# Optimization experiments

Measured on AMD Instinct MI355X. Metric: run time of the kernel, lower is better.

## Reference

```python
import jax, jax.numpy as jnp
import numpy as np

# irreps_in = irreps_out = 64x0e + 32x1o
MUL0, MUL1 = 64, 32          # multiplicities of 0e scalars and 1o vectors
DIM_IN = MUL0 + MUL1 * 3     # 160
N_NODES = 50000
IU0, IV0 = np.triu_indices(MUL0, k=1)   # 2016 scalar u<v pairs
IU1, IV1 = np.triu_indices(MUL1, k=1)   # 496 vector u<v pairs
# e3nn path normalization (component / element):
#   i_out=0 (0e): num_elements sum = 2016 + 64 + 496 + 32 = 2608, dim(0e)=1
#   i_out=1 (1o): num_elements = 32*64 = 2048, dim(1o)=3
C0 = float(np.sqrt(1.0 / 2608.0))
C1 = float(np.sqrt(3.0 / 2048.0))
INV_SQRT3 = float(1.0 / np.sqrt(3.0))   # w3j(1,0,1) and w3j(1,1,0) CG factor


def setup_inputs() -> dict:
    key = jax.random.key(0)
    ks = jax.random.split(key, 7)
    node_feats = jax.random.normal(ks[0], (N_NODES, DIM_IN), jnp.float32)
    node_messages = jax.random.normal(ks[1], (N_NODES, DIM_IN), jnp.float32)
    W1 = jax.random.normal(ks[2], (len(IU0), MUL0), jnp.float32)  # (0e,0e)->0e u<vw
    W2 = jax.random.normal(ks[3], (MUL0, MUL0), jnp.float32)      # (0e,0e)->0e uuw
    W3 = jax.random.normal(ks[4], (MUL1, MUL0, MUL1), jnp.float32)  # (1o,0e)->1o uvw
    W4 = jax.random.normal(ks[5], (len(IU1), MUL0), jnp.float32)  # (1o,1o)->0e u<vw
    W5 = jax.random.normal(ks[6], (MUL1, MUL0), jnp.float32)      # (1o,1o)->0e uuw
    return {"node_feats": node_feats, "node_messages": node_messages,
            "W1": W1, "W2": W2, "W3": W3, "W4": W4, "W5": W5}


def _tensor_square(x, W1, W2, W3, W4, W5):
    x0 = x[:, :MUL0]                        # [N, 64] scalars (0e)
    x1 = x[:, MUL0:].reshape(-1, MUL1, 3)   # [N, 32, 3] vectors (1o)
    # (0e x 0e) -> 0e
    pair0 = x0[:, IU0] * x0[:, IV0]         # [N, 2016]
    sq0 = x0 * x0                           # [N, 64]
    # (1o x 1o) -> 0e via dot products (w3j(1,1,0) = delta/sqrt3)
    d = jnp.einsum('nui,nvi->nuv', x1, x1)  # [N, 32, 32]
    pair1 = d[:, IU1, IV1] * INV_SQRT3      # [N, 496]
    diag1 = jnp.einsum('nui,nui->nu', x1, x1) * INV_SQRT3  # [N, 32]
    out0 = C0 * (pair0 @ W1 + sq0 @ W2 + pair1 @ W4 + diag1 @ W5)  # [N, 64]
    # (1o x 0e) -> 1o fully connected uvw (w3j(1,0,1) = eye/sqrt3)
    out1 = (C1 * INV_SQRT3) * jnp.einsum('nui,nv,uvw->nwi', x1, x0, W3)  # [N,32,3]
    return jnp.concatenate([out0, out1.reshape(-1, MUL1 * 3)], axis=1)


def reference(node_feats, node_messages, W1, W2, W3, W4, W5):
    x = node_feats + node_messages
    return _tensor_square(x, W1, W2, W3, W4, W5)
```

## Files before the change

### kernel.cpp

```cpp
#include <hip/hip_runtime.h>

typedef unsigned short u16;
typedef unsigned int u32;

#define N_NODES 50000
#define NB      32

#define BG_OFF  0
#define BT_OFF  262144
#define BH_OFF  327680

#define ASTR   72
#define XTSTR  36

typedef __attribute__((ext_vector_type(8))) short short8;
typedef __attribute__((ext_vector_type(4))) float f32x4;
union U4S8 { uint4 u; short8 s; };

__device__ __forceinline__ u16 f2bf(float f) {
    u32 u = __float_as_uint(f);
    return (u16)((u + 0x7fffu + ((u >> 16) & 1u)) >> 16);
}
__device__ __forceinline__ f32x4 bf4(uint2 q) {
    f32x4 r;
    r[0] = __uint_as_float(q.x << 16);
    r[1] = __uint_as_float(q.x & 0xffff0000u);
    r[2] = __uint_as_float(q.y << 16);
    r[3] = __uint_as_float(q.y & 0xffff0000u);
    return r;
}

__global__ __launch_bounds__(256)
void pack_kernel(const float* __restrict__ W1, const float* __restrict__ W2,
                 const float* __restrict__ W3, const float* __restrict__ W4,
                 const float* __restrict__ W5, u16* __restrict__ ws) {
    const float INV_SQRT3 = 0.57735026918962576f;
    int T = blockIdx.x * 256 + threadIdx.x;
    int slot0 = T * 8;
    float vals[8];
    if (slot0 < BT_OFF) {
        int ntile = slot0 >> 10, rem = slot0 & 1023;
        int ks = rem >> 9, q = (rem & 511) >> 3;
        int vbase = ks * 32 + (q >> 4) * 8;
        int j = ntile * 16 + (q & 15);
        int u = j >> 6, w = j & 63;
        #pragma unroll
        for (int jj = 0; jj < 8; ++jj) {
            int v = vbase + jj;
            if (v == u) vals[jj] = W2[u * 64 + w];
            else {
                int a = min(u, v), b = max(u, v);
                int p = a * (127 - a) / 2 + (b - a - 1);
                vals[jj] = 0.5f * W1[p * 64 + w];
            }
        }
    } else if (slot0 < BH_OFF) {
        int s = slot0 - BT_OFF;
        int ntile = s >> 10, rem = s & 1023;
        int ks = rem >> 9, q = (rem & 511) >> 3;
        int vbase = ks * 32 + (q >> 4) * 8;
        int j = ntile * 16 + (q & 15);
        int u = j >> 5, w = j & 31;
        #pragma unroll
        for (int jj = 0; jj < 8; ++jj)
            vals[jj] = W3[(u * 64 + (vbase + jj)) * 32 + w];
    } else {
        int s = slot0 - BH_OFF;
        int ntile = s >> 9, q = (s & 511) >> 3;
        int vbase = (q >> 4) * 8;
        int j = ntile * 16 + (q & 15);
        int u = j >> 6, w = j & 63;
        #pragma unroll
        for (int jj = 0; jj < 8; ++jj) {
            int v = vbase + jj;
            if (v == u) vals[jj] = W5[u * 64 + w] * INV_SQRT3;
            else {
                int a = min(u, v), b = max(u, v);
                int p = a * (63 - a) / 2 + (b - a - 1);
                vals[jj] = (0.5f * INV_SQRT3) * W4[p * 64 + w];
            }
        }
    }
    uint4 o;
    o.x = ((u32)f2bf(vals[1]) << 16) | f2bf(vals[0]);
    o.y = ((u32)f2bf(vals[3]) << 16) | f2bf(vals[2]);
    o.z = ((u32)f2bf(vals[5]) << 16) | f2bf(vals[4]);
    o.w = ((u32)f2bf(vals[7]) << 16) | f2bf(vals[6]);
    *(uint4*)(ws + slot0) = o;
}

__global__ __launch_bounds__(256, 3)
void node_block_kernel(const float* __restrict__ feats, const float* __restrict__ msgs,
                       const u16* __restrict__ ws, float* __restrict__ out) {
    __shared__ u16 A_S[32 * ASTR];
    __shared__ u16 x0T[64 * XTSTR];
    __shared__ u16 x1T[96 * XTSTR];

    const int tid = threadIdx.x;
    const int node0 = blockIdx.x * NB;

    for (int k = 0; k < 3; ++k) {
        int chunk = tid + k * 256;
        if (chunk < 640) {
            int idx = chunk * 8;
            int n = (u32)idx / 160u;
            int d = idx - n * 160;
            int g = node0 * 160 + idx;
            float v[8];
            if (g + 8 <= N_NODES * 160) {
                float4 fa0 = *(const float4*)(feats + g);
                float4 fa1 = *(const float4*)(feats + g + 4);
                float4 fb0 = *(const float4*)(msgs + g);
                float4 fb1 = *(const float4*)(msgs + g + 4);
                v[0]=fa0.x+fb0.x; v[1]=fa0.y+fb0.y; v[2]=fa0.z+fb0.z; v[3]=fa0.w+fb0.w;
                v[4]=fa1.x+fb1.x; v[5]=fa1.y+fb1.y; v[6]=fa1.z+fb1.z; v[7]=fa1.w+fb1.w;
            } else {
                #pragma unroll
                for (int j = 0; j < 8; ++j) v[j] = 0.f;
            }
            u16 bv[8];
            #pragma unroll
            for (int j = 0; j < 8; ++j) bv[j] = f2bf(v[j]);
            if (d < 64) {
                uint4 pk;
                pk.x = ((u32)bv[1] << 16) | bv[0];
                pk.y = ((u32)bv[3] << 16) | bv[2];
                pk.z = ((u32)bv[5] << 16) | bv[4];
                pk.w = ((u32)bv[7] << 16) | bv[6];
                *(uint4*)&A_S[n * ASTR + d] = pk;
                #pragma unroll
                for (int j = 0; j < 8; ++j) x0T[(d + j) * XTSTR + n] = bv[j];
            } else {
                #pragma unroll
                for (int j = 0; j < 8; ++j)
                    x1T[(d + j - 64) * XTSTR + n] = bv[j];
            }
        }
    }
    __syncthreads();

    const int wave = tid >> 6, lane = tid & 63, quad = lane >> 4, l15 = lane & 15;
    const int wq = wave;
    const f32x4 z4 = {0.f, 0.f, 0.f, 0.f};
    const int ph64 = (blockIdx.x * 5) & 63;
    const int ph32 = (blockIdx.x * 5) & 31;

    f32x4 o0[2];
    #pragma unroll
    for (int mt = 0; mt < 2; ++mt) o0[mt] = z4;

    {
        short8 aS[2][2];
        #pragma unroll
        for (int mt = 0; mt < 2; ++mt)
            #pragma unroll
            for (int ks = 0; ks < 2; ++ks) {
                U4S8 t; t.u = *(const uint4*)&A_S[(mt * 16 + l15) * ASTR + ks * 32 + quad * 8];
                aS[mt][ks] = t.s;
            }
        const u16* bp = ws + BG_OFF + (u32)wq * 1024 + lane * 8;
        U4S8 b0[2], b1[2];
        b0[0].u = *(const uint4*)(bp + ph64 * 4096);
        b1[0].u = *(const uint4*)(bp + ph64 * 4096 + 512);
        {
            int p1 = ((ph64 + 1) & 63) * 4096;
            b0[1].u = *(const uint4*)(bp + p1);
            b1[1].u = *(const uint4*)(bp + p1 + 512);
        }
        #pragma unroll 2
        for (int t = 0; t < 64; ++t) {
            const int c = t & 1;
            const int u = (ph64 + t) & 63;
            short8 B0 = b0[c].s, B1 = b1[c].s;
            {
                int pp = ((ph64 + t + 2) & 63) * 4096;
                b0[c].u = *(const uint4*)(bp + pp);
                b1[c].u = *(const uint4*)(bp + pp + 512);
            }
            f32x4 acc[2];
            #pragma unroll
            for (int mt = 0; mt < 2; ++mt) acc[mt] = z4;
            #pragma unroll
            for (int mt = 0; mt < 2; ++mt)
                acc[mt] = __builtin_amdgcn_mfma_f32_16x16x32_bf16(aS[mt][0], B0, acc[mt], 0, 0, 0);
            #pragma unroll
            for (int mt = 0; mt < 2; ++mt)
                acc[mt] = __builtin_amdgcn_mfma_f32_16x16x32_bf16(aS[mt][1], B1, acc[mt], 0, 0, 0);
            #pragma unroll
            for (int mt = 0; mt < 2; ++mt) {
                f32x4 xq = bf4(*(const uint2*)&x0T[u * XTSTR + mt * 16 + quad * 4]);
                o0[mt] += xq * acc[mt];
            }
        }
    }

    {
        short8 aH[6];
        #pragma unroll
        for (int i = 0; i < 3; ++i)
            #pragma unroll
            for (int m = 0; m < 2; ++m) {
                const int n = m * 16 + l15;
                union { short8 s; u16 e[8]; } t;
                #pragma unroll
                for (int j = 0; j < 8; ++j)
                    t.e[j] = x1T[((quad * 8 + j) * 3 + i) * XTSTR + n];
                aH[i * 2 + m] = t.s;
            }
        const u16* bp = ws + BH_OFF + (u32)wq * 512 + lane * 8;
        U4S8 bb[2];
        bb[0].u = *(const uint4*)(bp + ph32 * 2048);
        bb[1].u = *(const uint4*)(bp + ((ph32 + 1) & 31) * 2048);
        #pragma unroll 2
        for (int t = 0; t < 32; ++t) {
            const int c = t & 1;
            const int u = (ph32 + t) & 31;
            short8 B = bb[c].s;
            bb[c].u = *(const uint4*)(bp + ((ph32 + t + 2) & 31) * 2048);
            #pragma unroll
            for (int i = 0; i < 3; ++i) {
                f32x4 acc[2];
                #pragma unroll
                for (int m = 0; m < 2; ++m) acc[m] = z4;
                #pragma unroll
                for (int m = 0; m < 2; ++m)
                    acc[m] = __builtin_amdgcn_mfma_f32_16x16x32_bf16(aH[i * 2 + m], B, acc[m], 0, 0, 0);
                #pragma unroll
                for (int m = 0; m < 2; ++m) {
                    f32x4 xq = bf4(*(const uint2*)&x1T[(u * 3 + i) * XTSTR + m * 16 + quad * 4]);
                    o0[m] += xq * acc[m];
                }
            }
        }
    }

    {
        const float C0v = 0.019581512f;
        #pragma unroll
        for (int mt = 0; mt < 2; ++mt)
            #pragma unroll
            for (int rr = 0; rr < 4; ++rr) {
                int node = node0 + mt * 16 + quad * 4 + rr;
                if (node < N_NODES)
                    out[node * 160 + wq * 16 + l15] = C0v * o0[mt][rr];
            }
    }

    {
        const int mh = wave >> 1, wh = wave & 1;
        short8 aT[2];
        #pragma unroll
        for (int ks = 0; ks < 2; ++ks) {
            U4S8 t; t.u = *(const uint4*)&A_S[(mh * 16 + l15) * ASTR + ks * 32 + quad * 8];
            aT[ks] = t.s;
        }
        f32x4 o1[3];
        #pragma unroll
        for (int i = 0; i < 3; ++i) o1[i] = z4;

        const u16* bp = ws + BT_OFF + (u32)wh * 1024 + lane * 8;
        U4S8 b0[2], b1[2];
        b0[0].u = *(const uint4*)(bp + ph32 * 2048);
        b1[0].u = *(const uint4*)(bp + ph32 * 2048 + 512);
        {
            int p1 = ((ph32 + 1) & 31) * 2048;
            b0[1].u = *(const uint4*)(bp + p1);
            b1[1].u = *(const uint4*)(bp + p1 + 512);
        }
        #pragma unroll 2
        for (int t = 0; t < 32; ++t) {
            const int c = t & 1;
            const int u = (ph32 + t) & 31;
            short8 B0 = b0[c].s, B1 = b1[c].s;
            {
                int pp = ((ph32 + t + 2) & 31) * 2048;
                b0[c].u = *(const uint4*)(bp + pp);
                b1[c].u = *(const uint4*)(bp + pp + 512);
            }
            f32x4 acc = __builtin_amdgcn_mfma_f32_16x16x32_bf16(aT[0], B0, z4, 0, 0, 0);
            acc = __builtin_amdgcn_mfma_f32_16x16x32_bf16(aT[1], B1, acc, 0, 0, 0);
            #pragma unroll
            for (int i = 0; i < 3; ++i) {
                f32x4 xq = bf4(*(const uint2*)&x1T[(u * 3 + i) * XTSTR + mh * 16 + quad * 4]);
                o1[i] += xq * acc;
            }
        }
        const float S1 = 0.022097087f;
        #pragma unroll
        for (int i = 0; i < 3; ++i)
            #pragma unroll
            for (int rr = 0; rr < 4; ++rr) {
                int node = node0 + mh * 16 + quad * 4 + rr;
                if (node < N_NODES)
                    out[node * 160 + 64 + (wh * 16 + l15) * 3 + i] = S1 * o1[i][rr];
            }
    }
}

extern "C" void kernel_launch(void* const* d_in, const int* in_sizes, int n_in,
                              void* d_out, int out_size, void* d_ws, size_t ws_size,
                              hipStream_t stream) {
    const float* feats = (const float*)d_in[0];
    const float* msgs  = (const float*)d_in[1];
    const float* W1    = (const float*)d_in[2];
    const float* W2    = (const float*)d_in[3];
    const float* W3    = (const float*)d_in[4];
    const float* W4    = (const float*)d_in[5];
    const float* W5    = (const float*)d_in[6];
    float* out = (float*)d_out;
    u16* ws = (u16*)d_ws;

    hipLaunchKernelGGL(pack_kernel, dim3(192), dim3(256), 0, stream,
                       W1, W2, W3, W4, W5, ws);
    hipLaunchKernelGGL(node_block_kernel, dim3((N_NODES + NB - 1) / NB), dim3(256), 0, stream,
                       feats, msgs, ws, out);
}
```

Baseline: 181.1 us.

## Split u-loop across two wave groups with LDS reduction, 512-thread blocks

Doubles the block to 8 waves. The two groups of four waves each handle half of the u-range in all three contraction loops, and their partial accumulators are combined through new LDS buffers before the final store. The goal is more waves in flight per node block, so each wave's serial MFMA loop is shorter and latency is hidden better. The cost is extra LDS (red0/red1), two more barriers, and duplicated A-fragment loads in both wave groups.

```diff
diff --git a/kernel.cpp b/kernel.cpp
--- a/kernel.cpp
+++ b/kernel.cpp
@@ -12,6 +12,8 @@
 
 #define ASTR   72
 #define XTSTR  36
+#define R0STR  65
+#define R1STR  98
 
 typedef __attribute__((ext_vector_type(8))) short short8;
 typedef __attribute__((ext_vector_type(4))) float f32x4;
@@ -89,18 +91,20 @@
     *(uint4*)(ws + slot0) = o;
 }
 
-__global__ __launch_bounds__(256, 3)
+__global__ __launch_bounds__(512, 6)
 void node_block_kernel(const float* __restrict__ feats, const float* __restrict__ msgs,
                        const u16* __restrict__ ws, float* __restrict__ out) {
     __shared__ u16 A_S[32 * ASTR];
     __shared__ u16 x0T[64 * XTSTR];
     __shared__ u16 x1T[96 * XTSTR];
+    __shared__ float red0[32 * R0STR];
+    __shared__ float red1[32 * R1STR];
 
     const int tid = threadIdx.x;
     const int node0 = blockIdx.x * NB;
 
-    for (int k = 0; k < 3; ++k) {
-        int chunk = tid + k * 256;
+    for (int k = 0; k < 2; ++k) {
+        int chunk = tid + k * 512;
         if (chunk < 640) {
             int idx = chunk * 8;
             int n = (u32)idx / 160u;
@@ -140,10 +144,13 @@
     __syncthreads();
 
     const int wave = tid >> 6, lane = tid & 63, quad = lane >> 4, l15 = lane & 15;
-    const int wq = wave;
+    const int wq = wave & 3;
+    const int uh = wave >> 2;
     const f32x4 z4 = {0.f, 0.f, 0.f, 0.f};
     const int ph64 = (blockIdx.x * 5) & 63;
     const int ph32 = (blockIdx.x * 5) & 31;
+    const int ubS = ph64 + uh * 32;
+    const int ubH = ph32 + uh * 16;
 
     f32x4 o0[2];
     #pragma unroll
@@ -160,20 +167,20 @@
             }
         const u16* bp = ws + BG_OFF + (u32)wq * 1024 + lane * 8;
         U4S8 b0[2], b1[2];
-        b0[0].u = *(const uint4*)(bp + ph64 * 4096);
-        b1[0].u = *(const uint4*)(bp + ph64 * 4096 + 512);
+        b0[0].u = *(const uint4*)(bp + (ubS & 63) * 4096);
+        b1[0].u = *(const uint4*)(bp + (ubS & 63) * 4096 + 512);
         {
-            int p1 = ((ph64 + 1) & 63) * 4096;
+            int p1 = ((ubS + 1) & 63) * 4096;
             b0[1].u = *(const uint4*)(bp + p1);
             b1[1].u = *(const uint4*)(bp + p1 + 512);
         }
         #pragma unroll 2
-        for (int t = 0; t < 64; ++t) {
+        for (int t = 0; t < 32; ++t) {
             const int c = t & 1;
-            const int u = (ph64 + t) & 63;
+            const int u = (ubS + t) & 63;
             short8 B0 = b0[c].s, B1 = b1[c].s;
             {
-                int pp = ((ph64 + t + 2) & 63) * 4096;
+                int pp = ((ubS + t + 2) & 63) * 4096;
                 b0[c].u = *(const uint4*)(bp + pp);
                 b1[c].u = *(const uint4*)(bp + pp + 512);
             }
@@ -209,14 +216,14 @@
             }
         const u16* bp = ws + BH_OFF + (u32)wq * 512 + lane * 8;
         U4S8 bb[2];
-        bb[0].u = *(const uint4*)(bp + ph32 * 2048);
-        bb[1].u = *(const uint4*)(bp + ((ph32 + 1) & 31) * 2048);
+        bb[0].u = *(const uint4*)(bp + (ubH & 31) * 2048);
+        bb[1].u = *(const uint4*)(bp + ((ubH + 1) & 31) * 2048);
         #pragma unroll 2
-        for (int t = 0; t < 32; ++t) {
+        for (int t = 0; t < 16; ++t) {
             const int c = t & 1;
-            const int u = (ph32 + t) & 31;
+            const int u = (ubH + t) & 31;
             short8 B = bb[c].s;
-            bb[c].u = *(const uint4*)(bp + ((ph32 + t + 2) & 31) * 2048);
+            bb[c].u = *(const uint4*)(bp + ((ubH + t + 2) & 31) * 2048);
             #pragma unroll
             for (int i = 0; i < 3; ++i) {
                 f32x4 acc[2];
@@ -234,20 +241,29 @@
         }
     }
 
-    {
+    if (uh == 1) {
+        #pragma unroll
+        for (int mt = 0; mt < 2; ++mt)
+            #pragma unroll
+            for (int rr = 0; rr < 4; ++rr)
+                red0[(mt * 16 + quad * 4 + rr) * R0STR + wq * 16 + l15] = o0[mt][rr];
+    }
+    __syncthreads();
+    if (uh == 0) {
         const float C0v = 0.019581512f;
         #pragma unroll
         for (int mt = 0; mt < 2; ++mt)
             #pragma unroll
             for (int rr = 0; rr < 4; ++rr) {
+                float s = o0[mt][rr] + red0[(mt * 16 + quad * 4 + rr) * R0STR + wq * 16 + l15];
                 int node = node0 + mt * 16 + quad * 4 + rr;
                 if (node < N_NODES)
-                    out[node * 160 + wq * 16 + l15] = C0v * o0[mt][rr];
+                    out[node * 160 + wq * 16 + l15] = C0v * s;
             }
     }
 
     {
-        const int mh = wave >> 1, wh = wave & 1;
+        const int mh = (wave >> 1) & 1, wh = wave & 1;
         short8 aT[2];
         #pragma unroll
         for (int ks = 0; ks < 2; ++ks) {
@@ -260,20 +276,20 @@
 
         const u16* bp = ws + BT_OFF + (u32)wh * 1024 + lane * 8;
         U4S8 b0[2], b1[2];
-        b0[0].u = *(const uint4*)(bp + ph32 * 2048);
-        b1[0].u = *(const uint4*)(bp + ph32 * 2048 + 512);
+        b0[0].u = *(const uint4*)(bp + (ubH & 31) * 2048);
+        b1[0].u = *(const uint4*)(bp + (ubH & 31) * 2048 + 512);
         {
-            int p1 = ((ph32 + 1) & 31) * 2048;
+            int p1 = ((ubH + 1) & 31) * 2048;
             b0[1].u = *(const uint4*)(bp + p1);
             b1[1].u = *(const uint4*)(bp + p1 + 512);
         }
         #pragma unroll 2
-        for (int t = 0; t < 32; ++t) {
+        for (int t = 0; t < 16; ++t) {
             const int c = t & 1;
-            const int u = (ph32 + t) & 31;
+            const int u = (ubH + t) & 31;
             short8 B0 = b0[c].s, B1 = b1[c].s;
             {
-                int pp = ((ph32 + t + 2) & 31) * 2048;
+                int pp = ((ubH + t + 2) & 31) * 2048;
                 b0[c].u = *(const uint4*)(bp + pp);
                 b1[c].u = *(const uint4*)(bp + pp + 512);
             }
@@ -285,15 +301,27 @@
                 o1[i] += xq * acc;
             }
         }
-        const float S1 = 0.022097087f;
-        #pragma unroll
-        for (int i = 0; i < 3; ++i)
-            #pragma unroll
-            for (int rr = 0; rr < 4; ++rr) {
-                int node = node0 + mh * 16 + quad * 4 + rr;
-                if (node < N_NODES)
-                    out[node * 160 + 64 + (wh * 16 + l15) * 3 + i] = S1 * o1[i][rr];
-            }
+
+        if (uh == 1) {
+            #pragma unroll
+            for (int i = 0; i < 3; ++i)
+                #pragma unroll
+                for (int rr = 0; rr < 4; ++rr)
+                    red1[(mh * 16 + quad * 4 + rr) * R1STR + (wh * 16 + l15) * 3 + i] = o1[i][rr];
+        }
+        __syncthreads();
+        if (uh == 0) {
+            const float S1 = 0.022097087f;
+            #pragma unroll
+            for (int i = 0; i < 3; ++i)
+                #pragma unroll
+                for (int rr = 0; rr < 4; ++rr) {
+                    float s = o1[i][rr] + red1[(mh * 16 + quad * 4 + rr) * R1STR + (wh * 16 + l15) * 3 + i];
+                    int node = node0 + mh * 16 + quad * 4 + rr;
+                    if (node < N_NODES)
+                        out[node * 160 + 64 + (wh * 16 + l15) * 3 + i] = S1 * s;
+                }
+        }
     }
 }
 
@@ -312,6 +340,6 @@
 
     hipLaunchKernelGGL(pack_kernel, dim3(192), dim3(256), 0, stream,
                        W1, W2, W3, W4, W5, ws);
-    hipLaunchKernelGGL(node_block_kernel, dim3((N_NODES + NB - 1) / NB), dim3(256), 0, stream,
+    hipLaunchKernelGGL(node_block_kernel, dim3((N_NODES + NB - 1) / NB), dim3(512), 0, stream,
                        feats, msgs, ws, out);
 }
```

After: 183.7 us. No clear change (+1.4%).
